# Performance work log

Measured on AMD Instinct MI355X. Metric: run time of the kernel, lower is better.

The kernel has to match this reference:

```python
import jax, jax.numpy as jnp
import numpy as np

EPS_POS = 0.65
EPS_NEG = 0.4
TAU = 0.03
TEMPERATURE = 0.07


def setup_inputs() -> dict:
    key = jax.random.key(0)
    k1, k2 = jax.random.split(key)
    N, H, W, C = 256, 14, 14, 512  # ResNet18 layer4 features (448x448 frame), pooled audio
    frame = jax.random.normal(k1, (N, H, W, C), dtype=jnp.float32)
    audio = jax.random.normal(k2, (N, C), dtype=jnp.float32)
    return {"frame": frame, "audio": audio}


def reference(frame, audio):
    # frame: [N, H, W, C] vision backbone features; audio: [N, C] pooled audio embedding
    N = frame.shape[0]
    f = frame * jax.lax.rsqrt(jnp.sum(frame * frame, axis=3, keepdims=True))  # l2_normalize axis=3
    a = audio * jax.lax.rsqrt(jnp.sum(audio * audio, axis=1, keepdims=True))  # l2_normalize axis=1

    # S_ii: per-sample spatial similarity map [N, 1, H, W]
    S_ii = jnp.einsum('nhwc,nc->nhw', f, a)[:, None, :, :]
    # S_ij: cross-batch similarity [N, K, H, W] (K == N)
    S_ij = jnp.einsum('nhwc,kc->nkhw', f, a)

    m_ip = jax.nn.sigmoid((S_ii - EPS_POS) / TAU)   # positive soft-mask
    neg = 1.0 - jax.nn.sigmoid((S_ii - EPS_NEG) / TAU)  # hard-negative soft-mask

    # Pi: masked mean of positive similarities -> [N, 1]
    Pi = jnp.sum(m_ip * S_ii, axis=(2, 3)) / jnp.sum(m_ip, axis=(2, 3))

    n_all = jax.nn.sigmoid((S_ij - EPS_POS) / TAU)
    mask = 1.0 - 100.0 * jnp.eye(N, dtype=frame.dtype)  # kill diagonal (self) pairs
    Ni_easy = (jnp.sum(n_all * S_ij, axis=(2, 3)) / jnp.sum(n_all, axis=(2, 3))) * mask  # [N, N]
    Ni_hard = jnp.sum(neg * S_ii, axis=(2, 3)) / jnp.sum(neg, axis=(2, 3))  # [N, 1]

    data = jnp.concatenate([Pi, Ni_hard, Ni_easy], axis=1) * TEMPERATURE  # [N, N+2]

    # __calc_loss (faithful to TF broadcasting: Pi_d is [N,1], Ni_d is [N] -> [N,N] broadcast)
    Pi_d = data[:, 0:1]
    Ni_d = jnp.sum(data[:, 1:], axis=1)
    Pi_e = jnp.exp(Pi_d)
    Ni_e = jnp.exp(Ni_d)
    loss = (-1.0 / N) * jnp.sum(jnp.log(Pi_e / (Pi_e + Ni_e)))
    return loss
```

## Files before the change

### kernel.cpp

```cpp
#include <hip/hip_runtime.h>
#include <stdint.h>

#define N_IMG 256
#define HW 196
#define CDIM 512

#define F_EPS_POS 0.65f
#define F_EPS_NEG 0.40f
#define F_INV_TAU (1.0f/0.03f)
#define F_TEMP 0.07f

typedef __attribute__((ext_vector_type(8))) short bf16x8;
typedef __attribute__((ext_vector_type(4))) unsigned short u16x4;
typedef __attribute__((ext_vector_type(4))) float f32x4;

__device__ __forceinline__ unsigned short f2bf(float x){
    unsigned int u = __float_as_uint(x);
    u = (u + 0x7FFFu + ((u >> 16) & 1u)) >> 16;
    return (unsigned short)u;
}
__device__ __forceinline__ float sigm(float x){ return 1.0f/(1.0f + __expf(-x)); }

__global__ void audio_norm_k(const float* __restrict__ audio,
                             unsigned short* __restrict__ abf){
    int k = blockIdx.x, t = threadIdx.x;
    __shared__ float red[256];
    float v0 = audio[k*CDIM + t];
    float v1 = audio[k*CDIM + t + 256];
    red[t] = v0*v0 + v1*v1;
    __syncthreads();
    for (int s = 128; s > 0; s >>= 1){
        if (t < s) red[t] += red[t+s];
        __syncthreads();
    }
    float rrt = 1.0f / sqrtf(red[0]);
    abf[k*CDIM + t]       = f2bf(v0*rrt);
    abf[k*CDIM + t + 256] = f2bf(v1*rrt);
}

__global__ __launch_bounds__(512, 2)
void main_k(const float* __restrict__ frame,
            const unsigned short* __restrict__ abf,
            float* __restrict__ num, float* __restrict__ den,
            float* __restrict__ hnum, float* __restrict__ hden){
    __shared__ unsigned short fT[2][16*520];
    __shared__ float rnormS[2][16];

    const int t    = threadIdx.x;
    const int n    = blockIdx.x;
    const int lane = t & 63, wid = t >> 6;
    const int col  = lane & 15, quad = lane >> 4;
    const int kg0  = wid*32 + col;
    const int kg1  = kg0 + 16;

    bf16x8 B0[16], B1[16];
    {
        const unsigned short* b0p = abf + (size_t)kg0*CDIM + quad*8;
        const unsigned short* b1p = abf + (size_t)kg1*CDIM + quad*8;
        #pragma unroll
        for (int j = 0; j < 16; ++j){
            B0[j] = *(const bf16x8*)(b0p + j*32);
            B1[j] = *(const bf16x8*)(b1p + j*32);
        }
    }

    const int r0 = 2*wid, r1 = r0 + 1;

    float en0=0.f, en1=0.f, ed0=0.f, ed1=0.f;
    float hn0=0.f, hn1=0.f, hd0=0.f, hd1=0.f;

    auto loadT = [&](int pt, float4* v){
        int p0 = pt*16 + r0; if (p0 > HW-1) p0 = HW-1;
        int p1 = pt*16 + r1; if (p1 > HW-1) p1 = HW-1;
        const float4* s0 = (const float4*)(frame + ((size_t)n*HW + p0)*CDIM);
        const float4* s1 = (const float4*)(frame + ((size_t)n*HW + p1)*CDIM);
        v[0] = s0[lane]; v[1] = s0[lane + 64];
        v[2] = s1[lane]; v[3] = s1[lane + 64];
    };
    auto storeT = [&](const float4* v, int buf){
        float ss0 = v[0].x*v[0].x + v[0].y*v[0].y + v[0].z*v[0].z + v[0].w*v[0].w
                  + v[1].x*v[1].x + v[1].y*v[1].y + v[1].z*v[1].z + v[1].w*v[1].w;
        float ss1 = v[2].x*v[2].x + v[2].y*v[2].y + v[2].z*v[2].z + v[2].w*v[2].w
                  + v[3].x*v[3].x + v[3].y*v[3].y + v[3].z*v[3].z + v[3].w*v[3].w;
        unsigned short* d0 = fT[buf] + r0*520;
        unsigned short* d1 = fT[buf] + r1*520;
        u16x4 u0 = { f2bf(v[0].x), f2bf(v[0].y), f2bf(v[0].z), f2bf(v[0].w) };
        u16x4 u1 = { f2bf(v[1].x), f2bf(v[1].y), f2bf(v[1].z), f2bf(v[1].w) };
        u16x4 u2 = { f2bf(v[2].x), f2bf(v[2].y), f2bf(v[2].z), f2bf(v[2].w) };
        u16x4 u3 = { f2bf(v[3].x), f2bf(v[3].y), f2bf(v[3].z), f2bf(v[3].w) };
        *(u16x4*)(d0 + lane*4)       = u0;
        *(u16x4*)(d0 + 256 + lane*4) = u1;
        *(u16x4*)(d1 + lane*4)       = u2;
        *(u16x4*)(d1 + 256 + lane*4) = u3;
        #pragma unroll
        for (int d = 1; d < 64; d <<= 1){
            ss0 += __shfl_xor(ss0, d, 64);
            ss1 += __shfl_xor(ss1, d, 64);
        }
        if (lane == 0){
            rnormS[buf][r0] = (ss0 > 0.f) ? (1.0f/sqrtf(ss0)) : 0.f;
            rnormS[buf][r1] = (ss1 > 0.f) ? (1.0f/sqrtf(ss1)) : 0.f;
        }
    };

    {
        float4 v[4];
        loadT(0, v);
        storeT(v, 0);
    }
    __syncthreads();

    for (int pt = 0; pt < 13; ++pt){
        const int cur = pt & 1, nxt = cur ^ 1;
        const bool hasNext = (pt < 12);

        float4 v[4];
        if (hasNext) loadT(pt + 1, v);

        const unsigned short* fbase = fT[cur] + col*520 + quad*8;
        f32x4 acc0 = {0.f,0.f,0.f,0.f};
        f32x4 acc1 = {0.f,0.f,0.f,0.f};
        #pragma unroll
        for (int j = 0; j < 16; ++j){
            bf16x8 a = *(const bf16x8*)(fbase + j*32);
            acc0 = __builtin_amdgcn_mfma_f32_16x16x32_bf16(a, B0[j], acc0, 0, 0, 0);
            acc1 = __builtin_amdgcn_mfma_f32_16x16x32_bf16(a, B1[j], acc1, 0, 0, 0);
        }
        f32x4 rn4 = *(const f32x4*)(&rnormS[cur][quad*4]);
        #pragma unroll
        for (int rr = 0; rr < 4; ++rr){
            int prow = pt*16 + quad*4 + rr;
            if (prow < HW){
                float s0 = acc0[rr] * rn4[rr];
                float s1 = acc1[rr] * rn4[rr];
                float w0 = sigm((s0 - F_EPS_POS) * F_INV_TAU);
                float w1 = sigm((s1 - F_EPS_POS) * F_INV_TAU);
                en0 += w0*s0; ed0 += w0;
                en1 += w1*s1; ed1 += w1;
                if (kg0 == n){ float wn = 1.f - sigm((s0 - F_EPS_NEG) * F_INV_TAU); hn0 += wn*s0; hd0 += wn; }
                if (kg1 == n){ float wn = 1.f - sigm((s1 - F_EPS_NEG) * F_INV_TAU); hn1 += wn*s1; hd1 += wn; }
            }
        }

        if (hasNext) storeT(v, nxt);
        __syncthreads();
    }

    en0 += __shfl_xor(en0, 16, 64); en0 += __shfl_xor(en0, 32, 64);
    ed0 += __shfl_xor(ed0, 16, 64); ed0 += __shfl_xor(ed0, 32, 64);
    en1 += __shfl_xor(en1, 16, 64); en1 += __shfl_xor(en1, 32, 64);
    ed1 += __shfl_xor(ed1, 16, 64); ed1 += __shfl_xor(ed1, 32, 64);
    hn0 += __shfl_xor(hn0, 16, 64); hn0 += __shfl_xor(hn0, 32, 64);
    hd0 += __shfl_xor(hd0, 16, 64); hd0 += __shfl_xor(hd0, 32, 64);
    hn1 += __shfl_xor(hn1, 16, 64); hn1 += __shfl_xor(hn1, 32, 64);
    hd1 += __shfl_xor(hd1, 16, 64); hd1 += __shfl_xor(hd1, 32, 64);

    if (quad == 0){
        num[n*N_IMG + kg0] = en0;  den[n*N_IMG + kg0] = ed0;
        num[n*N_IMG + kg1] = en1;  den[n*N_IMG + kg1] = ed1;
        if (kg0 == n){ hnum[n] = hn0; hden[n] = hd0; }
        if (kg1 == n){ hnum[n] = hn1; hden[n] = hd1; }
    }
}

__global__ void pd_k(const float* __restrict__ num, const float* __restrict__ den,
                     const float* __restrict__ hnum, const float* __restrict__ hden,
                     float* __restrict__ Pi_d, float* __restrict__ Ni_d){
    int nn = blockIdx.x, t = threadIdx.x;
    __shared__ float red[256];
    __shared__ float diagv;
    float ratio = num[nn*N_IMG + t] / den[nn*N_IMG + t];
    if (t == nn) diagv = ratio;
    red[t] = ratio * (t == nn ? -99.f : 1.f);
    __syncthreads();
    for (int s = 128; s > 0; s >>= 1){
        if (t < s) red[t] += red[t+s];
        __syncthreads();
    }
    if (t == 0){
        Pi_d[nn] = F_TEMP * diagv;
        Ni_d[nn] = F_TEMP * (hnum[nn]/hden[nn] + red[0]);
    }
}

__global__ void loss_k(const float* __restrict__ Pi_d, const float* __restrict__ Ni_d,
                       float* __restrict__ out){
    int i = blockIdx.x, j = threadIdx.x;
    __shared__ float red[256];
    float x = Ni_d[j] - Pi_d[i];
    red[j] = (x > 20.f) ? x : log1pf(__expf(x));
    __syncthreads();
    for (int s = 128; s > 0; s >>= 1){
        if (j < s) red[j] += red[j+s];
        __syncthreads();
    }
    if (j == 0) atomicAdd(out, red[0] * (1.0f/(float)N_IMG));
}

extern "C" void kernel_launch(void* const* d_in, const int* in_sizes, int n_in,
                              void* d_out, int out_size, void* d_ws, size_t ws_size,
                              hipStream_t stream) {
    const float* frame = (const float*)d_in[0];
    const float* audio = (const float*)d_in[1];
    float* out = (float*)d_out;
    char* ws = (char*)d_ws;

    unsigned short* abf = (unsigned short*)(ws);
    float* num  = (float*)(ws + 262144);
    float* den  = (float*)(ws + 524288);
    float* hnum = (float*)(ws + 786432);
    float* hden = (float*)(ws + 787456);
    float* Pi_d = (float*)(ws + 788480);
    float* Ni_d = (float*)(ws + 789504);

    hipMemsetAsync(out, 0, sizeof(float), stream);

    audio_norm_k<<<N_IMG, 256, 0, stream>>>(audio, abf);
    main_k<<<N_IMG, 512, 0, stream>>>(frame, abf, num, den, hnum, hden);
    pd_k<<<N_IMG, 256, 0, stream>>>(num, den, hnum, hden, Pi_d, Ni_d);
    loss_k<<<N_IMG, 256, 0, stream>>>(Pi_d, Ni_d, out);
}
```

Baseline: 175.9 us.

## Restructure main GEMM to loop over K chunks with full-spatial accumulators in registers

The kernel previously held the whole audio B matrix in registers and looped over 16-row spatial tiles. It now loops over 16 chunks of 32 channels, staging both frame rows (all 208 padded) and the audio chunk in padded LDS double buffers, and keeps 26 accumulator tiles per wave across the full spatial extent. Row norms are accumulated across chunks and applied after the GEMM. The aim is to free the large B register footprint and use narrower, more coalesced loads, at the cost of many accumulator registers, more LDS, and dropping the 2-blocks-per-CU launch bound, which can lower occupancy.

```diff
diff --git a/kernel.cpp b/kernel.cpp
--- a/kernel.cpp
+++ b/kernel.cpp
@@ -4,6 +4,9 @@
 #define N_IMG 256
 #define HW 196
 #define CDIM 512
+#define NCH 16
+#define AROWS 208
+#define LSTR 40
 
 #define F_EPS_POS 0.65f
 #define F_EPS_NEG 0.40f
@@ -11,7 +14,6 @@
 #define F_TEMP 0.07f
 
 typedef __attribute__((ext_vector_type(8))) short bf16x8;
-typedef __attribute__((ext_vector_type(4))) unsigned short u16x4;
 typedef __attribute__((ext_vector_type(4))) float f32x4;
 
 __device__ __forceinline__ unsigned short f2bf(float x){
@@ -38,13 +40,14 @@
     abf[k*CDIM + t + 256] = f2bf(v1*rrt);
 }
 
-__global__ __launch_bounds__(512, 2)
+__global__ __launch_bounds__(512)
 void main_k(const float* __restrict__ frame,
             const unsigned short* __restrict__ abf,
             float* __restrict__ num, float* __restrict__ den,
             float* __restrict__ hnum, float* __restrict__ hden){
-    __shared__ unsigned short fT[2][16*520];
-    __shared__ float rnormS[2][16];
+    __shared__ __align__(16) unsigned short Ash[2][AROWS*LSTR];
+    __shared__ __align__(16) unsigned short Bsh[2][N_IMG*LSTR];
+    __shared__ __align__(16) float rnS[AROWS];
 
     const int t    = threadIdx.x;
     const int n    = blockIdx.x;
@@ -53,86 +56,94 @@
     const int kg0  = wid*32 + col;
     const int kg1  = kg0 + 16;
 
-    bf16x8 B0[16], B1[16];
-    {
-        const unsigned short* b0p = abf + (size_t)kg0*CDIM + quad*8;
-        const unsigned short* b1p = abf + (size_t)kg1*CDIM + quad*8;
-        #pragma unroll
-        for (int j = 0; j < 16; ++j){
-            B0[j] = *(const bf16x8*)(b0p + j*32);
-            B1[j] = *(const bf16x8*)(b1p + j*32);
-        }
-    }
-
-    const int r0 = 2*wid, r1 = r0 + 1;
+    const int rw = t >> 4;
+    const int c8 = t & 15;
+    const int bk = t >> 1;
+    const int bh = t & 1;
+
+    float  ss[7] = {0.f,0.f,0.f,0.f,0.f,0.f,0.f};
+    float2 va[7];
+    uint4  vb[2];
+
+    auto loadC = [&](int ch){
+        #pragma unroll
+        for (int i = 0; i < 7; ++i){
+            int row  = i*32 + rw;
+            int prow = (row > HW-1) ? HW-1 : row;
+            va[i] = *(const float2*)(frame + ((size_t)n*HW + prow)*CDIM
+                                     + ch*32 + c8*2);
+        }
+        const unsigned short* bp = abf + bk*CDIM + ch*32 + bh*16;
+        vb[0] = *(const uint4*)(bp);
+        vb[1] = *(const uint4*)(bp + 8);
+    };
+    auto storeC = [&](int buf){
+        #pragma unroll
+        for (int i = 0; i < 7; ++i){
+            int row = i*32 + rw;
+            if (row < AROWS){
+                float x = va[i].x, y = va[i].y;
+                if (row < HW) ss[i] += x*x + y*y;
+                unsigned int pk = (unsigned int)f2bf(x)
+                                | ((unsigned int)f2bf(y) << 16);
+                *(unsigned int*)((char*)&Ash[buf][row*LSTR] + c8*4) = pk;
+            }
+        }
+        *(uint4*)((char*)&Bsh[buf][bk*LSTR] + bh*32)      = vb[0];
+        *(uint4*)((char*)&Bsh[buf][bk*LSTR] + bh*32 + 16) = vb[1];
+    };
+
+    f32x4 acc0[13], acc1[13];
+    #pragma unroll
+    for (int f = 0; f < 13; ++f){
+        acc0[f] = (f32x4){0.f,0.f,0.f,0.f};
+        acc1[f] = (f32x4){0.f,0.f,0.f,0.f};
+    }
+
+    loadC(0); storeC(0);
+    __syncthreads();
+
+    for (int s = 0; s < NCH; ++s){
+        if (s < NCH-1) loadC(s + 1);
+        __builtin_amdgcn_sched_barrier(0);
+        const int cur = s & 1;
+        bf16x8 b0 = *(const bf16x8*)((char*)&Bsh[cur][(wid*32 + col)*LSTR] + quad*16);
+        bf16x8 b1 = *(const bf16x8*)((char*)&Bsh[cur][(wid*32 + 16 + col)*LSTR] + quad*16);
+        #pragma unroll
+        for (int f = 0; f < 13; ++f){
+            bf16x8 a = *(const bf16x8*)((char*)&Ash[cur][(f*16 + col)*LSTR] + quad*16);
+            acc0[f] = __builtin_amdgcn_mfma_f32_16x16x32_bf16(a, b0, acc0[f], 0, 0, 0);
+            acc1[f] = __builtin_amdgcn_mfma_f32_16x16x32_bf16(a, b1, acc1[f], 0, 0, 0);
+        }
+        if (s < NCH-1) storeC((s + 1) & 1);
+        __syncthreads();
+    }
+
+    if (t < AROWS - HW) rnS[HW + t] = 0.f;
+    #pragma unroll
+    for (int i = 0; i < 7; ++i){
+        float sv = ss[i];
+        sv += __shfl_xor(sv, 1, 64);
+        sv += __shfl_xor(sv, 2, 64);
+        sv += __shfl_xor(sv, 4, 64);
+        sv += __shfl_xor(sv, 8, 64);
+        int row = i*32 + rw;
+        if (c8 == 0 && row < HW)
+            rnS[row] = (sv > 0.f) ? (1.0f/sqrtf(sv)) : 0.f;
+    }
+    __syncthreads();
 
     float en0=0.f, en1=0.f, ed0=0.f, ed1=0.f;
     float hn0=0.f, hn1=0.f, hd0=0.f, hd1=0.f;
-
-    auto loadT = [&](int pt, float4* v){
-        int p0 = pt*16 + r0; if (p0 > HW-1) p0 = HW-1;
-        int p1 = pt*16 + r1; if (p1 > HW-1) p1 = HW-1;
-        const float4* s0 = (const float4*)(frame + ((size_t)n*HW + p0)*CDIM);
-        const float4* s1 = (const float4*)(frame + ((size_t)n*HW + p1)*CDIM);
-        v[0] = s0[lane]; v[1] = s0[lane + 64];
-        v[2] = s1[lane]; v[3] = s1[lane + 64];
-    };
-    auto storeT = [&](const float4* v, int buf){
-        float ss0 = v[0].x*v[0].x + v[0].y*v[0].y + v[0].z*v[0].z + v[0].w*v[0].w
-                  + v[1].x*v[1].x + v[1].y*v[1].y + v[1].z*v[1].z + v[1].w*v[1].w;
-        float ss1 = v[2].x*v[2].x + v[2].y*v[2].y + v[2].z*v[2].z + v[2].w*v[2].w
-                  + v[3].x*v[3].x + v[3].y*v[3].y + v[3].z*v[3].z + v[3].w*v[3].w;
-        unsigned short* d0 = fT[buf] + r0*520;
-        unsigned short* d1 = fT[buf] + r1*520;
-        u16x4 u0 = { f2bf(v[0].x), f2bf(v[0].y), f2bf(v[0].z), f2bf(v[0].w) };
-        u16x4 u1 = { f2bf(v[1].x), f2bf(v[1].y), f2bf(v[1].z), f2bf(v[1].w) };
-        u16x4 u2 = { f2bf(v[2].x), f2bf(v[2].y), f2bf(v[2].z), f2bf(v[2].w) };
-        u16x4 u3 = { f2bf(v[3].x), f2bf(v[3].y), f2bf(v[3].z), f2bf(v[3].w) };
-        *(u16x4*)(d0 + lane*4)       = u0;
-        *(u16x4*)(d0 + 256 + lane*4) = u1;
-        *(u16x4*)(d1 + lane*4)       = u2;
-        *(u16x4*)(d1 + 256 + lane*4) = u3;
-        #pragma unroll
-        for (int d = 1; d < 64; d <<= 1){
-            ss0 += __shfl_xor(ss0, d, 64);
-            ss1 += __shfl_xor(ss1, d, 64);
-        }
-        if (lane == 0){
-            rnormS[buf][r0] = (ss0 > 0.f) ? (1.0f/sqrtf(ss0)) : 0.f;
-            rnormS[buf][r1] = (ss1 > 0.f) ? (1.0f/sqrtf(ss1)) : 0.f;
-        }
-    };
-
-    {
-        float4 v[4];
-        loadT(0, v);
-        storeT(v, 0);
-    }
-    __syncthreads();
-
-    for (int pt = 0; pt < 13; ++pt){
-        const int cur = pt & 1, nxt = cur ^ 1;
-        const bool hasNext = (pt < 12);
-
-        float4 v[4];
-        if (hasNext) loadT(pt + 1, v);
-
-        const unsigned short* fbase = fT[cur] + col*520 + quad*8;
-        f32x4 acc0 = {0.f,0.f,0.f,0.f};
-        f32x4 acc1 = {0.f,0.f,0.f,0.f};
-        #pragma unroll
-        for (int j = 0; j < 16; ++j){
-            bf16x8 a = *(const bf16x8*)(fbase + j*32);
-            acc0 = __builtin_amdgcn_mfma_f32_16x16x32_bf16(a, B0[j], acc0, 0, 0, 0);
-            acc1 = __builtin_amdgcn_mfma_f32_16x16x32_bf16(a, B1[j], acc1, 0, 0, 0);
-        }
-        f32x4 rn4 = *(const f32x4*)(&rnormS[cur][quad*4]);
+    #pragma unroll
+    for (int f = 0; f < 13; ++f){
+        f32x4 rn4 = *(const f32x4*)(&rnS[f*16 + quad*4]);
         #pragma unroll
         for (int rr = 0; rr < 4; ++rr){
-            int prow = pt*16 + quad*4 + rr;
-            if (prow < HW){
-                float s0 = acc0[rr] * rn4[rr];
-                float s1 = acc1[rr] * rn4[rr];
+            int pr = f*16 + quad*4 + rr;
+            if (pr < HW){
+                float s0 = acc0[f][rr] * rn4[rr];
+                float s1 = acc1[f][rr] * rn4[rr];
                 float w0 = sigm((s0 - F_EPS_POS) * F_INV_TAU);
                 float w1 = sigm((s1 - F_EPS_POS) * F_INV_TAU);
                 en0 += w0*s0; ed0 += w0;
@@ -141,9 +152,6 @@
                 if (kg1 == n){ float wn = 1.f - sigm((s1 - F_EPS_NEG) * F_INV_TAU); hn1 += wn*s1; hd1 += wn; }
             }
         }
-
-        if (hasNext) storeT(v, nxt);
-        __syncthreads();
     }
 
     en0 += __shfl_xor(en0, 16, 64); en0 += __shfl_xor(en0, 32, 64);
```

Result: slower. 219.0 us (+24.5%).
